# Kernel optimization log

Measured on AMD Instinct MI355X. Metric: run time of the kernel, lower is better.

## Reference

```python
import jax, jax.numpy as jnp
import numpy as np

B_CHUNK = 5          # hardcoded self.B in the module
GAMMA = 0.9865
BATCH, SEQ, FEAT, DIM = 8, 4000, 256, 256


def setup_inputs() -> dict:
    key = jax.random.key(0)
    ks = jax.random.split(key, 6)
    xq = jax.random.normal(ks[0], (BATCH, SEQ, FEAT), jnp.float32)
    xk = jax.random.normal(ks[1], (BATCH, SEQ, FEAT), jnp.float32)
    xv = jax.random.normal(ks[2], (BATCH, SEQ, FEAT), jnp.float32)
    scale = 1.0 / np.sqrt(FEAT).astype(np.float32)
    Wq = jax.random.normal(ks[3], (FEAT, DIM), jnp.float32) * scale
    Wk = jax.random.normal(ks[4], (FEAT, DIM), jnp.float32) * scale
    Wv = jax.random.normal(ks[5], (FEAT, DIM), jnp.float32) * scale
    return {"xq": xq, "xk": xk, "xv": xv, "Wq": Wq, "Wk": Wk, "Wv": Wv}


def reference(xq, xk, xv, Wq, Wk, Wv):
    gamma = jnp.float32(GAMMA)
    B = B_CHUNK
    b, seq, _ = xq.shape
    dim = Wq.shape[1]
    n = seq // B  # number of chunks

    # projections, chunked: [b, n, B, dim]
    Q = (xq @ Wq).reshape(b, n, B, dim)
    K = (xk @ Wk).reshape(b, n, B, dim)
    V = (xv @ Wv).reshape(b, n, B, dim)

    chunk_idx = jnp.arange(n, dtype=jnp.float32)
    # Z[i] = gamma^(B - i - 1) (per-chunk scalar, as in original)
    Z = gamma ** (jnp.float32(B) - chunk_idx - 1.0)
    Vz = V * Z[None, :, None, None]

    # intra-chunk decay matrix: L[i,j] = gamma^(j-i) for i >= j, else 0
    pos = jnp.arange(B, dtype=jnp.float32)
    L = jnp.tril(gamma ** (pos[None, :] - pos[:, None]))

    # intra-chunk term: (Q K^T * L) @ V, vectorized over all chunks
    S = jnp.einsum('bnid,bnjd->bnij', Q, K)          # [b, n, B, B]
    intra = jnp.einsum('bnij,bnjd->bnid', S * L, V)  # [b, n, B, dim]

    # cross-chunk recurrence: R[i] = K_i^T Vz_i + gamma^B R[i-1]
    # X[i-1] += Q_i @ R[i-1] * gamma^(i+1)
    Qn = jnp.moveaxis(Q, 1, 0)   # [n, b, B, dim]
    Kn = jnp.moveaxis(K, 1, 0)
    Vzn = jnp.moveaxis(Vz, 1, 0)
    gB = gamma ** B

    def step(R_prev, inp):
        qi, ki, vzi, i = inp
        cross_prev = jnp.einsum('bod,bde->boe', qi, R_prev) * gamma ** (i + 1.0)
        R_new = jnp.einsum('bod,boe->bde', ki, vzi) + gB * R_prev
        return R_new, cross_prev

    R0 = jnp.zeros((b, dim, dim), xq.dtype)
    _, ys = jax.lax.scan(step, R0, (Qn, Kn, Vzn, chunk_idx))  # ys[i] = cross for chunk i-1
    cross = jnp.concatenate([ys[1:], jnp.zeros_like(ys[:1])], axis=0)  # last chunk has no cross term
    cross = jnp.moveaxis(cross, 0, 1)  # [b, n, B, dim]

    X = intra + cross
    return X.reshape(b, seq, dim)
```

## Files before the change

### kernel.cpp

```cpp
#include <hip/hip_runtime.h>
#include <cmath>

#define GAMMA 0.9865f
#define L2G   -0.01960905f
#define BATCH 8
#define SEQ   4000
#define CSUP  25
#define GSUP  32
#define RPG   125

typedef _Float16 half8 __attribute__((ext_vector_type(8)));
typedef _Float16 half4 __attribute__((ext_vector_type(4)));
typedef float    floatx4 __attribute__((ext_vector_type(4)));

__device__ __forceinline__ float gpow(float e) { return exp2f(e * L2G); }

__global__ __launch_bounds__(256) void wt_convert(
    const float* __restrict__ Wq, const float* __restrict__ Wk, const float* __restrict__ Wv,
    _Float16* __restrict__ Wt) {
    int t = blockIdx.x * 256 + threadIdx.x;
    int mat = t >> 16, rem = t & 65535;
    int n = rem >> 8, k = rem & 255;
    const float* W = (mat == 0) ? Wq : (mat == 1) ? Wk : Wv;
    Wt[(size_t)mat * 65536 + n * 256 + k] = (_Float16)W[k * 256 + n];
}

__global__ __launch_bounds__(256, 2) void qkv_gemm_f16(
    const float* __restrict__ xq, const float* __restrict__ xk, const float* __restrict__ xv,
    const _Float16* __restrict__ WtAll,
    _Float16* __restrict__ Qb, _Float16* __restrict__ Kb, _Float16* __restrict__ Vb) {
    int op = blockIdx.y;
    const float* x = (op == 0) ? xq : (op == 1) ? xk : xv;
    const _Float16* Wt = WtAll + (size_t)op * 65536;
    _Float16* dst = (op == 0) ? Qb : (op == 1) ? Kb : Vb;

    __shared__ _Float16 Xs[2][128][40];
    __shared__ _Float16 WsT[2][256][40];

    int t = threadIdx.x;
    int lane = t & 63, wave = t >> 6;
    int ln = lane & 15, q8 = (lane >> 4) << 3, q4 = (lane >> 4) << 2;
    int row0 = blockIdx.x * 128;

    int xm = t >> 3, xk_ = (t & 7) << 2;
    int wr = t >> 2, wk = (t & 3) << 3;

    floatx4 acc[8][4] = {};
    floatx4 xn[4]; half8 wn[4];

    auto loadNext = [&](int dt) {
        int k0 = dt * 32;
#pragma unroll
        for (int i = 0; i < 4; ++i)
            xn[i] = *(const floatx4*)&x[(size_t)(row0 + xm + i * 32) * 256 + k0 + xk_];
#pragma unroll
        for (int i = 0; i < 4; ++i)
            wn[i] = *(const half8*)&Wt[(wr + i * 64) * 256 + k0 + wk];
    };
    auto writeBuf = [&](int bf) {
#pragma unroll
        for (int i = 0; i < 4; ++i) {
            half4 h; h[0] = (_Float16)xn[i][0]; h[1] = (_Float16)xn[i][1];
            h[2] = (_Float16)xn[i][2]; h[3] = (_Float16)xn[i][3];
            *(half4*)&Xs[bf][xm + i * 32][xk_] = h;
        }
#pragma unroll
        for (int i = 0; i < 4; ++i)
            *(half8*)&WsT[bf][wr + i * 64][wk] = wn[i];
    };

    loadNext(0); writeBuf(0);
    int cur = 0;
    for (int dt = 0; dt < 8; ++dt) {
        __syncthreads();
        if (dt < 7) loadNext(dt + 1);
        half8 af[8];
#pragma unroll
        for (int mi = 0; mi < 8; ++mi) af[mi] = *(const half8*)&Xs[cur][mi * 16 + ln][q8];
#pragma unroll
        for (int ni = 0; ni < 4; ++ni) {
            half8 bf = *(const half8*)&WsT[cur][(wave * 4 + ni) * 16 + ln][q8];
#pragma unroll
            for (int mi = 0; mi < 8; ++mi)
                acc[mi][ni] = __builtin_amdgcn_mfma_f32_16x16x32_f16(af[mi], bf, acc[mi][ni], 0, 0, 0);
        }
        if (dt < 7) { writeBuf(cur ^ 1); cur ^= 1; }
    }
#pragma unroll
    for (int mi = 0; mi < 8; ++mi)
#pragma unroll
        for (int ni = 0; ni < 4; ++ni)
#pragma unroll
            for (int r = 0; r < 4; ++r) {
                int row = row0 + mi * 16 + q4 + r;
                int col = (wave * 4 + ni) * 16 + ln;
                dst[(size_t)row * 256 + col] = (_Float16)acc[mi][ni][r];
            }
}

__global__ __launch_bounds__(256) void vt_transpose(
    const _Float16* __restrict__ Vb, _Float16* __restrict__ VT) {
    int es = blockIdx.x, g = blockIdx.y, b = blockIdx.z;
    int t = threadIdx.x;
    __shared__ __align__(16) _Float16 Ls[64 * 136];
#pragma unroll
    for (int i = 0; i < 4; ++i) {
        int idx = t + i * 256;
        int cp = idx >> 3, eg = idx & 7;
        half8 v = {};
        if (cp < 125)
            v = *(const half8*)&Vb[((size_t)b * SEQ + g * RPG + cp) * 256 + es * 64 + eg * 8];
        int cpg = cp >> 3, c7 = cp & 7;
#pragma unroll
        for (int z = 0; z < 8; ++z) {
            int e = eg * 8 + z;
            Ls[e * 136 + ((cpg ^ (e >> 3)) << 3) + c7] = v[z];
        }
    }
    __syncthreads();
#pragma unroll
    for (int jj = 0; jj < 4; ++jj) {
        int ee = jj * 16 + (t >> 4);
        int cpg = t & 15;
        half8 h = *(const half8*)&Ls[ee * 136 + ((cpg ^ (ee >> 3)) << 3)];
        *(half8*)&VT[(((size_t)b * 256 + es * 64 + ee) * 32 + g) * 128 + cpg * 8] = h;
    }
}

__global__ __launch_bounds__(256, 2) void chunk_states_mfma(
    const _Float16* __restrict__ Kb, const _Float16* __restrict__ Vb,
    _Float16* __restrict__ Wh) {
    int lin = blockIdx.x + 2 * (blockIdx.y + 32 * blockIdx.z);
    int swz = (lin & 7) * 64 + (lin >> 3);
    int eh = swz & 1, g = (swz >> 1) & 31, b = swz >> 6;

    int t = threadIdx.x, lane = t & 63, wave = t >> 6;
    int ln = lane & 15, q8 = (lane >> 4) << 3, q4 = (lane >> 4) << 2;
    __shared__ __align__(16) _Float16 VsT[128 * 40];
    __shared__ __align__(16) _Float16 KsT[256 * 40];
    size_t base_row = (size_t)b * SEQ + g * RPG;
    floatx4 acc[8][4] = {};
    int rb = q8 >> 3;
    for (int kt = 0; kt < 4; ++kt) {
        int r0 = kt * 32;
#pragma unroll
        for (int i = 0; i < 2; ++i) {
            int idx = t + i * 256;
            int r = idx >> 4, e8 = (idx & 15) << 3;
            half8 v = {};
            if (r0 + r < RPG) {
                v = *(const half8*)&Vb[(base_row + r0 + r) * 256 + eh * 128 + e8];
                int mloc = (r0 + r) / 5;
                float a = gpow((float)(149 - 6 * mloc));
#pragma unroll
                for (int z = 0; z < 8; ++z) v[z] = (_Float16)((float)v[z] * a);
            }
            int base = e8 * 40 + ((((r >> 3) ^ ((e8 >> 3) & 3))) << 3) + (r & 7);
#pragma unroll
            for (int z = 0; z < 8; ++z) VsT[base + z * 40] = v[z];
        }
#pragma unroll
        for (int i = 0; i < 4; ++i) {
            int idx = t + i * 256;
            int r = idx >> 5, d8 = (idx & 31) << 3;
            half8 v = {};
            if (r0 + r < RPG) v = *(const half8*)&Kb[(base_row + r0 + r) * 256 + d8];
            int base = d8 * 40 + ((((r >> 3) ^ ((d8 >> 3) & 3))) << 3) + (r & 7);
#pragma unroll
            for (int z = 0; z < 8; ++z) KsT[base + z * 40] = v[z];
        }
        __syncthreads();
        half8 Af[8], Bf[4];
#pragma unroll
        for (int mi = 0; mi < 8; ++mi) {
            int e = mi * 16 + ln;
            Af[mi] = *(const half8*)&VsT[e * 40 + ((rb ^ ((e >> 3) & 3)) << 3)];
        }
#pragma unroll
        for (int ni = 0; ni < 4; ++ni) {
            int d = wave * 64 + ni * 16 + ln;
            Bf[ni] = *(const half8*)&KsT[d * 40 + ((rb ^ ((d >> 3) & 3)) << 3)];
        }
#pragma unroll
        for (int mi = 0; mi < 8; ++mi)
#pragma unroll
            for (int ni = 0; ni < 4; ++ni)
                acc[mi][ni] = __builtin_amdgcn_mfma_f32_16x16x32_f16(Af[mi], Bf[ni], acc[mi][ni], 0, 0, 0);
        __syncthreads();
    }
    size_t ob = ((size_t)(g * 8 + b)) << 16;
#pragma unroll
    for (int mi = 0; mi < 8; ++mi)
#pragma unroll
        for (int ni = 0; ni < 4; ++ni)
#pragma unroll
            for (int r = 0; r < 4; ++r) {
                int e = eh * 128 + mi * 16 + q4 + r;
                int d = wave * 64 + ni * 16 + ln;
                Wh[ob + (size_t)e * 256 + d] = (_Float16)acc[mi][ni][r];
            }
}

__global__ __launch_bounds__(256) void state_scan(
    const _Float16* __restrict__ Wh, _Float16* __restrict__ SprevT) {
    int t = blockIdx.x * 256 + threadIdx.x;
    int b = t >> 14;
    int idx = (t & 16383) << 2;
    const float gF = gpow(150.0f);
    float s[4] = {};
    half4 w = *(const half4*)&Wh[(((size_t)b) << 16) + idx];
    for (int g = 0; g < GSUP; ++g) {
        size_t o = (((size_t)(g * 8 + b)) << 16) + idx;
        half4 wn = {};
        if (g < GSUP - 1) wn = *(const half4*)&Wh[o + (8ull << 16)];
        half4 sv;
#pragma unroll
        for (int z = 0; z < 4; ++z) { sv[z] = (_Float16)s[z]; s[z] = (float)w[z] + gF * s[z]; }
        *(half4*)&SprevT[o] = sv;
        w = wn;
    }
}

__global__ __launch_bounds__(256) void intra_sc(
    const _Float16* __restrict__ Qb, const _Float16* __restrict__ Kb, float* __restrict__ scw) {
    int b = blockIdx.y;
    int j = blockIdx.x * 4 + (threadIdx.x >> 6);
    int lane = threadIdx.x & 63;
    size_t base = ((size_t)b * SEQ + j * 5) * 256 + lane * 4;
    half4 qv[5], kv[5];
#pragma unroll
    for (int p = 0; p < 5; ++p) {
        qv[p] = *(const half4*)&Qb[base + p * 256];
        kv[p] = *(const half4*)&Kb[base + p * 256];
    }
#pragma unroll
    for (int p = 0; p < 5; ++p)
#pragma unroll
        for (int q = 0; q <= p; ++q) {
            float s = 0.f;
#pragma unroll
            for (int z = 0; z < 4; ++z) s += (float)qv[p][z] * (float)kv[q][z];
#pragma unroll
            for (int off = 32; off; off >>= 1) s += __shfl_xor(s, off, 64);
            if (lane == 0) scw[((size_t)b * 800 + j) * 25 + p * 5 + q] = s * gpow((float)(q - p));
        }
}

__global__ __launch_bounds__(512, 2) void cross_f16(
    const _Float16* __restrict__ Qb, const _Float16* __restrict__ Kb,
    const _Float16* __restrict__ VT, const _Float16* __restrict__ SprevT,
    const float* __restrict__ scw, float* __restrict__ out) {
    int lin = blockIdx.x + 4 * (blockIdx.y + 32 * blockIdx.z);
    int swz = (lin & 7) * 128 + (lin >> 3);
    int eq = swz & 3, g = (swz >> 2) & 31, b = swz >> 7;
    int e0 = eq * 64;
    int t = threadIdx.x;
    int lane = t & 63, wave = t >> 6;
    int ln = lane & 15, q8 = (lane >> 4) << 3, q4 = (lane >> 4) << 2;
    int mw = wave;

    __shared__ __align__(16) char smem[52224];
    _Float16* QsB  = (_Float16*)smem;
    _Float16* KsB  = (_Float16*)(smem + 20480);
    _Float16* SsB  = (_Float16*)(smem + 40960);
    _Float16* VsTB = (_Float16*)smem;
    _Float16* PsB  = (_Float16*)(smem + 17408);
#define QS(bf_, m_, k_)  QsB[(bf_) * 5120 + (m_) * 40 + (k_)]
#define KS(bf_, m_, k_)  KsB[(bf_) * 5120 + (m_) * 40 + (k_)]
#define SS(bf_, m_, k_)  SsB[(bf_) * 2560 + (m_) * 40 + (k_)]
#define PS(m_, k_)  PsB[(m_) * 136 + (k_)]
#define VST(m_, k_) VsTB[(m_) * 136 + (k_)]

    size_t kvbase = (size_t)b * SEQ + g * RPG;
    size_t sb = ((size_t)(g * 8 + b)) << 16;

    int qm = t >> 2, qk = (t & 3) << 3;
    int vm = t >> 3, vc = t & 7;

    floatx4 pacc[8] = {};
    floatx4 acc[4] = {};
    half8 qn, kn, sn;
    half8 vtp[2];

    auto loadNext = [&](int dt) {
        int d0 = dt * 32;
        half8 z = {};
        int qr = g * RPG + 5 + qm;
        qn = z;
        if (qm < 125 && qr < SEQ) qn = *(const half8*)&Qb[((size_t)b * SEQ + qr) * 256 + d0 + qk];
        kn = z;
        if (qm < 125) kn = *(const half8*)&Kb[(kvbase + qm) * 256 + d0 + qk];
        if (t < 256) sn = *(const half8*)&SprevT[sb + (size_t)(e0 + (t >> 2)) * 256 + d0 + qk];
    };
    auto writeBuf = [&](int bf) {
        *(half8*)&QS(bf, qm, qk) = qn;
        *(half8*)&KS(bf, qm, qk) = kn;
        if (t < 256) *(half8*)&SS(bf, t >> 2, qk) = sn;
    };

    loadNext(0); writeBuf(0);
    int cur = 0;
    for (int dt = 0; dt < 8; ++dt) {
        __syncthreads();
        if (dt < 7) loadNext(dt + 1);
        if (dt == 7) {
            size_t vtbase = (((size_t)b * 256 + e0 + vm) * 32 + g) * 128;
            vtp[0] = *(const half8*)&VT[vtbase + vc * 8];
            vtp[1] = *(const half8*)&VT[vtbase + (vc + 8) * 8];
        }
        half8 af = *(const half8*)&QS(cur, mw * 16 + ln, q8);
#pragma unroll
        for (int ci = 0; ci < 8; ++ci) {
            half8 bf = *(const half8*)&KS(cur, ci * 16 + ln, q8);
            pacc[ci] = __builtin_amdgcn_mfma_f32_16x16x32_f16(af, bf, pacc[ci], 0, 0, 0);
        }
#pragma unroll
        for (int ei = 0; ei < 4; ++ei) {
            half8 sf = *(const half8*)&SS(cur, ei * 16 + ln, q8);
            acc[ei] = __builtin_amdgcn_mfma_f32_16x16x32_f16(af, sf, acc[ei], 0, 0, 0);
        }
        if (dt < 7) { writeBuf(cur ^ 1); cur ^= 1; }
    }

#pragma unroll
    for (int r = 0; r < 4; ++r) {
        int rp = mw * 16 + q4 + r;
        int rc = rp / 5;
        float rs = 0.f;
        if (rp < 125 && !(g == GSUP - 1 && rc == CSUP - 1)) rs = gpow((float)(6 * rc + 7));
#pragma unroll
        for (int ei = 0; ei < 4; ++ei) acc[ei][r] *= rs;
    }

    __syncthreads();

    *(half8*)&VST(vm, vc << 3) = vtp[0];
    *(half8*)&VST(vm, (vc + 8) << 3) = vtp[1];
#pragma unroll
    for (int ci = 0; ci < 8; ++ci)
#pragma unroll
        for (int r = 0; r < 4; ++r) {
            int rp = mw * 16 + q4 + r;
            int cp = ci * 16 + ln;
            int rc = rp / 5, cc = cp / 5;
            float w = 0.f;
            if (rp < 125 && cp < 125 && cc <= rc && !(g == GSUP - 1 && rc == CSUP - 1))
                w = gpow((float)(6 * (rc - cc + 1)));
            PS(rp, cp) = (_Float16)(pacc[ci][r] * w);
        }
    __syncthreads();

#pragma unroll
    for (int ct = 0; ct < 4; ++ct) {
        int cp0 = ct * 32;
        half8 paf = *(const half8*)&PS(mw * 16 + ln, cp0 + q8);
#pragma unroll
        for (int ei = 0; ei < 4; ++ei) {
            half8 bv = *(const half8*)&VST(ei * 16 + ln, cp0 + q8);
            acc[ei] = __builtin_amdgcn_mfma_f32_16x16x32_f16(paf, bv, acc[ei], 0, 0, 0);
        }
    }

#pragma unroll
    for (int r = 0; r < 4; ++r) {
        int rp = mw * 16 + q4 + r;
        if (rp < 125) {
            int rc = rp / 5, pp = rp - rc * 5;
            const float* srow = scw + ((size_t)b * 800 + g * 25 + rc) * 25 + pp * 5;
            float a[4];
#pragma unroll
            for (int ei = 0; ei < 4; ++ei) a[ei] = acc[ei][r];
            for (int q = 0; q <= pp; ++q) {
                float s = srow[q];
#pragma unroll
                for (int ei = 0; ei < 4; ++ei)
                    a[ei] += s * (float)VST(ei * 16 + ln, rc * 5 + q);
            }
            size_t orow = ((size_t)b * SEQ + g * RPG + rp) * 256;
#pragma unroll
            for (int ei = 0; ei < 4; ++ei)
                out[orow + e0 + ei * 16 + ln] = a[ei];
        }
    }
}

extern "C" void kernel_launch(void* const* d_in, const int* in_sizes, int n_in,
                              void* d_out, int out_size, void* d_ws, size_t ws_size,
                              hipStream_t stream) {
    const float* xq = (const float*)d_in[0];
    const float* xk = (const float*)d_in[1];
    const float* xv = (const float*)d_in[2];
    const float* Wq = (const float*)d_in[3];
    const float* Wk = (const float*)d_in[4];
    const float* Wv = (const float*)d_in[5];
    float* out = (float*)d_out;

    const size_t NELEM = (size_t)SEQ * BATCH * 256;
    _Float16* Qb = (_Float16*)d_ws;
    _Float16* Kb = Qb + NELEM;
    _Float16* Vb = Kb + NELEM;
    _Float16* Wt = Vb + NELEM;
    _Float16* Wh = Wt + 196608;
    _Float16* SprevT = Wh + (size_t)GSUP * BATCH * 65536;
    float* scw = (float*)(SprevT + (size_t)GSUP * BATCH * 65536);
    _Float16* VT = Wh;

    wt_convert<<<dim3(768), 256, 0, stream>>>(Wq, Wk, Wv, Wt);
    qkv_gemm_f16<<<dim3(250, 3), 256, 0, stream>>>(xq, xk, xv, Wt, Qb, Kb, Vb);
    chunk_states_mfma<<<dim3(2, 32, 8), 256, 0, stream>>>(Kb, Vb, Wh);
    state_scan<<<dim3(512), 256, 0, stream>>>(Wh, SprevT);
    vt_transpose<<<dim3(4, 32, 8), 256, 0, stream>>>(Vb, VT);
    intra_sc<<<dim3(200, 8), 256, 0, stream>>>(Qb, Kb, scw);
    cross_f16<<<dim3(4, 32, 8), 512, 0, stream>>>(Qb, Kb, VT, SprevT, scw, out);
}
```

Measured before the change: 244.4 us.

## Stage QKV GEMM tiles via direct global-to-LDS loads with XOR swizzle

The QKV projection GEMM now copies X (kept in fp32) and W tiles straight from global memory into LDS with global_load_lds. This replaces the old path of loading into registers, converting, and then storing to LDS. XOR swizzled layouts replace the padded arrays to avoid bank conflicts, and the fp32-to-fp16 conversion of X moves to fragment-read time. The goal is to cut register pressure and VGPR round-trips during staging and to simplify the double buffer to one barrier per k-step. The trade-offs are that the fp32 X tile doubles its LDS footprint and that conversion work is repeated per fragment read.

Measured after the change: 242.7 us. No clear change (-0.7%).

```diff
diff --git a/kernel.cpp b/kernel.cpp
--- a/kernel.cpp
+++ b/kernel.cpp
@@ -14,6 +14,12 @@
 typedef float    floatx4 __attribute__((ext_vector_type(4)));
 
 __device__ __forceinline__ float gpow(float e) { return exp2f(e * L2G); }
+
+__device__ __forceinline__ void gl16(const void* g, void* l) {
+    __builtin_amdgcn_global_load_lds(
+        (const __attribute__((address_space(1))) void*)g,
+        (__attribute__((address_space(3))) void*)l, 16, 0, 0);
+}
 
 __global__ __launch_bounds__(256) void wt_convert(
     const float* __restrict__ Wq, const float* __restrict__ Wk, const float* __restrict__ Wv,
@@ -34,57 +40,65 @@
     const _Float16* Wt = WtAll + (size_t)op * 65536;
     _Float16* dst = (op == 0) ? Qb : (op == 1) ? Kb : Vb;
 
-    __shared__ _Float16 Xs[2][128][40];
-    __shared__ _Float16 WsT[2][256][40];
+    __shared__ __align__(16) float    XsF[2][128 * 32];
+    __shared__ __align__(16) _Float16 Ws[2][256 * 32];
 
     int t = threadIdx.x;
     int lane = t & 63, wave = t >> 6;
     int ln = lane & 15, q8 = (lane >> 4) << 3, q4 = (lane >> 4) << 2;
     int row0 = blockIdx.x * 128;
 
-    int xm = t >> 3, xk_ = (t & 7) << 2;
-    int wr = t >> 2, wk = (t & 3) << 3;
-
     floatx4 acc[8][4] = {};
-    floatx4 xn[4]; half8 wn[4];
-
-    auto loadNext = [&](int dt) {
+
+    auto stage = [&](int bf, int dt) {
         int k0 = dt * 32;
 #pragma unroll
-        for (int i = 0; i < 4; ++i)
-            xn[i] = *(const floatx4*)&x[(size_t)(row0 + xm + i * 32) * 256 + k0 + xk_];
-#pragma unroll
-        for (int i = 0; i < 4; ++i)
-            wn[i] = *(const half8*)&Wt[(wr + i * 64) * 256 + k0 + wk];
+        for (int i = 0; i < 4; ++i) {
+            int idx = t + i * 256;
+            int row = idx >> 3, p = idx & 7, c = p ^ (row & 7);
+            gl16(&x[(size_t)(row0 + row) * 256 + k0 + c * 4],
+                 (char*)&XsF[bf][0] + idx * 16);
+        }
+#pragma unroll
+        for (int i = 0; i < 4; ++i) {
+            int idx = t + i * 256;
+            int n = idx >> 2, p = idx & 3, c = p ^ ((n >> 1) & 3);
+            gl16(&Wt[n * 256 + k0 + c * 8],
+                 (char*)&Ws[bf][0] + idx * 16);
+        }
     };
-    auto writeBuf = [&](int bf) {
-#pragma unroll
-        for (int i = 0; i < 4; ++i) {
-            half4 h; h[0] = (_Float16)xn[i][0]; h[1] = (_Float16)xn[i][1];
-            h[2] = (_Float16)xn[i][2]; h[3] = (_Float16)xn[i][3];
-            *(half4*)&Xs[bf][xm + i * 32][xk_] = h;
-        }
-#pragma unroll
-        for (int i = 0; i < 4; ++i)
-            *(half8*)&WsT[bf][wr + i * 64][wk] = wn[i];
-    };
-
-    loadNext(0); writeBuf(0);
+
+    stage(0, 0);
+    __syncthreads();
     int cur = 0;
     for (int dt = 0; dt < 8; ++dt) {
-        __syncthreads();
-        if (dt < 7) loadNext(dt + 1);
+        if (dt < 7) stage(cur ^ 1, dt + 1);
         half8 af[8];
 #pragma unroll
-        for (int mi = 0; mi < 8; ++mi) af[mi] = *(const half8*)&Xs[cur][mi * 16 + ln][q8];
+        for (int mi = 0; mi < 8; ++mi) {
+            int row = mi * 16 + ln;
+            int s = ln & 7, c0 = q8 >> 2;
+            const float* base = &XsF[cur][row * 32];
+            floatx4 v0 = *(const floatx4*)&base[(c0 ^ s) << 2];
+            floatx4 v1 = *(const floatx4*)&base[((c0 + 1) ^ s) << 2];
+            half8 h;
+            h[0] = (_Float16)v0[0]; h[1] = (_Float16)v0[1];
+            h[2] = (_Float16)v0[2]; h[3] = (_Float16)v0[3];
+            h[4] = (_Float16)v1[0]; h[5] = (_Float16)v1[1];
+            h[6] = (_Float16)v1[2]; h[7] = (_Float16)v1[3];
+            af[mi] = h;
+        }
 #pragma unroll
         for (int ni = 0; ni < 4; ++ni) {
-            half8 bf = *(const half8*)&WsT[cur][(wave * 4 + ni) * 16 + ln][q8];
+            int n = (wave * 4 + ni) * 16 + ln;
+            int p = (q8 >> 3) ^ ((n >> 1) & 3);
+            half8 bf = *(const half8*)&Ws[cur][n * 32 + p * 8];
 #pragma unroll
             for (int mi = 0; mi < 8; ++mi)
                 acc[mi][ni] = __builtin_amdgcn_mfma_f32_16x16x32_f16(af[mi], bf, acc[mi][ni], 0, 0, 0);
         }
-        if (dt < 7) { writeBuf(cur ^ 1); cur ^= 1; }
+        __syncthreads();
+        cur ^= 1;
     }
 #pragma unroll
     for (int mi = 0; mi < 8; ++mi)
```
